# Optimization experiments

Hardware: AMD Instinct MI355X
Metric: run time of the kernel (lower is better)

Reference implementation:

```python
import jax, jax.numpy as jnp
import numpy as np

N1_SRC = 1171456  # hop-1 source nodes
N1_TGT = 45056    # hop-1 target nodes (= hop-2 source nodes)
N2_TGT = 4096     # final batch of target nodes
E1 = 1126400
E2 = 40960
IN_C, HID_C, OUT_C = 128, 256, 64


def setup_inputs() -> dict:
    key = jax.random.key(0)
    ks = jax.random.split(key, 12)
    inp = {
        "x": jax.random.normal(ks[0], (N1_SRC, IN_C), jnp.float32),
        "Wl1": jax.random.normal(ks[1], (IN_C, HID_C), jnp.float32) * (IN_C ** -0.5),
        "Wr1": jax.random.normal(ks[2], (IN_C, HID_C), jnp.float32) * (IN_C ** -0.5),
        "b1": jax.random.normal(ks[3], (HID_C,), jnp.float32) * 0.01,
        "Wl2": jax.random.normal(ks[4], (HID_C, OUT_C), jnp.float32) * (HID_C ** -0.5),
        "Wr2": jax.random.normal(ks[5], (HID_C, OUT_C), jnp.float32) * (HID_C ** -0.5),
        "b2": jax.random.normal(ks[6], (OUT_C,), jnp.float32) * 0.01,
        "src1": jax.random.randint(ks[7], (E1,), 0, N1_SRC, jnp.int32),
        "dst1": jax.random.randint(ks[8], (E1,), 0, N1_TGT, jnp.int32),
        "src2": jax.random.randint(ks[9], (E2,), 0, N1_TGT, jnp.int32),
        "dst2": jax.random.randint(ks[10], (E2,), 0, N2_TGT, jnp.int32),
    }
    return inp


def _sage_conv(x_src, x_tgt, src, dst, Wl, Wr, b, n_tgt):
    # mean aggregation of neighbor (source) features per target node
    msgs = x_src[src]                                   # [E, C] gather
    s = jax.ops.segment_sum(msgs, dst, num_segments=n_tgt)
    cnt = jax.ops.segment_sum(jnp.ones((src.shape[0],), x_src.dtype), dst,
                              num_segments=n_tgt)
    agg = s / jnp.maximum(cnt, 1.0)[:, None]
    # PyG SAGEConv: lin_l(aggregated) + lin_r(root), bias on lin_l
    return agg @ Wl + x_tgt @ Wr + b


def reference(x, Wl1, Wr1, b1, Wl2, Wr2, b2, src1, dst1, src2, dst2):
    # layer 0
    h = _sage_conv(x, x[:N1_TGT], src1, dst1, Wl1, Wr1, b1, N1_TGT)
    h = jax.nn.relu(h)  # dropout is identity in eval mode
    # layer 1
    out = _sage_conv(h, h[:N2_TGT], src2, dst2, Wl2, Wr2, b2, N2_TGT)
    return jax.nn.log_softmax(out, axis=-1)
```

## Files before the change

### kernel.cpp

```cpp
#include <hip/hip_runtime.h>
#include <hip/hip_bf16.h>

constexpr int N1_SRC = 1171456;
constexpr int N1_TGT = 45056;
constexpr int N2_TGT = 4096;
constexpr int E1 = 1126400;
constexpr int E2 = 40960;
constexpr int IN_C = 128;
constexpr int HID_C = 256;
constexpr int OUT_C = 64;

__global__ __launch_bounds__(256) void hist(const int* __restrict__ dst,
                                            int* __restrict__ cnt, int E) {
  const int i = blockIdx.x * blockDim.x + threadIdx.x;
  if (i < E) atomicAdd(&cnt[dst[i]], 1);
}

__global__ __launch_bounds__(1024) void scan_excl(const int* __restrict__ cnt,
                                                  int* __restrict__ off, int n) {
  const int tid = threadIdx.x;
  const int lane = tid & 63;
  const int wv = tid >> 6;
  __shared__ int wsum[16];
  __shared__ int carry_s;
  if (tid == 0) carry_s = 0;
  __syncthreads();
  for (int base = 0; base < n; base += 1024) {
    const int i = base + tid;
    const int v = (i < n) ? cnt[i] : 0;
    int s = v;
#pragma unroll
    for (int o = 1; o < 64; o <<= 1) {
      const int t = __shfl_up(s, o);
      if (lane >= o) s += t;
    }
    if (lane == 63) wsum[wv] = s;
    __syncthreads();
    if (wv == 0 && lane < 16) {
      const int ws = wsum[lane];
      int ss = ws;
#pragma unroll
      for (int o = 1; o < 16; o <<= 1) {
        const int t = __shfl_up(ss, o);
        if (lane >= o) ss += t;
      }
      wsum[lane] = ss - ws;
    }
    __syncthreads();
    const int excl = carry_s + wsum[wv] + (s - v);
    if (i < n) off[i] = excl;
    __syncthreads();
    if (tid == 1023) carry_s += wsum[15] + s;
    __syncthreads();
  }
}

__global__ __launch_bounds__(256) void fill_csr(
    const int* __restrict__ src, const int* __restrict__ dst,
    const int* __restrict__ off, int* __restrict__ cur,
    int* __restrict__ eidx, int E) {
  const int i = blockIdx.x * blockDim.x + threadIdx.x;
  if (i < E) {
    const int d = dst[i];
    const int p = atomicAdd(&cur[d], 1);
    eidx[off[d] + p] = src[i];
  }
}

template <int C>
__global__ __launch_bounds__(C) void gather_mean(
    const float* __restrict__ x, const int* __restrict__ eidx,
    const int* __restrict__ off, const int* __restrict__ cnt,
    float* __restrict__ agg) {
  const int node = blockIdx.x;
  const int c = threadIdx.x;
  const int beg = off[node];
  const int deg = cnt[node];
  float s0 = 0.f, s1 = 0.f, s2 = 0.f, s3 = 0.f;
  int i = 0;
  for (; i + 4 <= deg; i += 4) {
    const int n0 = eidx[beg + i + 0];
    const int n1 = eidx[beg + i + 1];
    const int n2 = eidx[beg + i + 2];
    const int n3 = eidx[beg + i + 3];
    s0 += x[(size_t)n0 * C + c];
    s1 += x[(size_t)n1 * C + c];
    s2 += x[(size_t)n2 * C + c];
    s3 += x[(size_t)n3 * C + c];
  }
  for (; i < deg; ++i) s0 += x[(size_t)eidx[beg + i] * C + c];
  const float s = (s0 + s1) + (s2 + s3);
  agg[(size_t)node * C + c] = s / (float)(deg > 0 ? deg : 1);
}

constexpr int BM = 64, BN = 64, BK = 16;
__global__ __launch_bounds__(256) void l1_dense(
    const float* __restrict__ agg1, const float* __restrict__ x,
    const float* __restrict__ Wl1, const float* __restrict__ Wr1,
    const float* __restrict__ b1, float* __restrict__ h) {
  __shared__ float As[BK][BM + 4];
  __shared__ float Bs[BK][BN + 4];
  const int br = blockIdx.x;
  const int bn = blockIdx.y;
  const int tid = threadIdx.x;
  const int tx = tid & 15;
  const int ty = tid >> 4;
  const int r0 = br * BM;
  const int n0 = bn * BN + tx * 4;

  float acc[4][4];
#pragma unroll
  for (int i = 0; i < 4; ++i)
#pragma unroll
    for (int j = 0; j < 4; ++j) acc[i][j] = b1[n0 + j];

  const int lr = tid >> 2;
  const int lk = (tid & 3) * 4;
  const int bk_ = tid >> 4;
  const int bn_ = (tid & 15) * 4;

  for (int phase = 0; phase < 2; ++phase) {
    const float* __restrict__ A = phase ? x : agg1;
    const float* __restrict__ W = phase ? Wr1 : Wl1;
    for (int k0 = 0; k0 < IN_C; k0 += BK) {
      const float4 av =
          *reinterpret_cast<const float4*>(A + (size_t)(r0 + lr) * IN_C + k0 + lk);
      As[lk + 0][lr] = av.x;
      As[lk + 1][lr] = av.y;
      As[lk + 2][lr] = av.z;
      As[lk + 3][lr] = av.w;
      const float4 wv = *reinterpret_cast<const float4*>(
          W + (size_t)(k0 + bk_) * HID_C + bn * BN + bn_);
      *reinterpret_cast<float4*>(&Bs[bk_][bn_]) = wv;
      __syncthreads();
#pragma unroll
      for (int k = 0; k < BK; ++k) {
        float a[4], b[4];
        *reinterpret_cast<float4*>(a) =
            *reinterpret_cast<const float4*>(&As[k][ty * 4]);
        *reinterpret_cast<float4*>(b) =
            *reinterpret_cast<const float4*>(&Bs[k][tx * 4]);
#pragma unroll
        for (int i = 0; i < 4; ++i)
#pragma unroll
          for (int j = 0; j < 4; ++j) acc[i][j] += a[i] * b[j];
      }
      __syncthreads();
    }
  }
#pragma unroll
  for (int i = 0; i < 4; ++i) {
    float4 o;
    o.x = fmaxf(acc[i][0], 0.0f);
    o.y = fmaxf(acc[i][1], 0.0f);
    o.z = fmaxf(acc[i][2], 0.0f);
    o.w = fmaxf(acc[i][3], 0.0f);
    *reinterpret_cast<float4*>(h + (size_t)(r0 + ty * 4 + i) * HID_C + n0) = o;
  }
}

__global__ __launch_bounds__(256) void l2_dense_lsm(
    const float* __restrict__ agg2, const float* __restrict__ h,
    const float* __restrict__ Wl2, const float* __restrict__ Wr2,
    const float* __restrict__ b2, float* __restrict__ out) {
  __shared__ float Aa[4][HID_C];
  __shared__ float Ax[4][HID_C];
  const int tid = threadIdx.x;
  const int rb = blockIdx.x * 4;
  const int lr = tid >> 6;
  const int lk = (tid & 63) * 4;
  const float4 sa =
      *reinterpret_cast<const float4*>(agg2 + (size_t)(rb + lr) * HID_C + lk);
  *reinterpret_cast<float4*>(&Aa[lr][lk]) = sa;
  const float4 xa =
      *reinterpret_cast<const float4*>(h + (size_t)(rb + lr) * HID_C + lk);
  *reinterpret_cast<float4*>(&Ax[lr][lk]) = xa;
  __syncthreads();

  const int r = tid >> 6;
  const int n = tid & 63;
  float acc = b2[n];
#pragma unroll 4
  for (int k = 0; k < HID_C; ++k) {
    acc += Aa[r][k] * Wl2[k * OUT_C + n];
    acc += Ax[r][k] * Wr2[k * OUT_C + n];
  }
  float m = acc;
#pragma unroll
  for (int o = 32; o; o >>= 1) m = fmaxf(m, __shfl_xor(m, o));
  const float e = expf(acc - m);
  float ssum = e;
#pragma unroll
  for (int o = 32; o; o >>= 1) ssum += __shfl_xor(ssum, o);
  out[(size_t)(rb + r) * OUT_C + n] = acc - m - logf(ssum);
}

extern "C" void kernel_launch(void* const* d_in, const int* in_sizes, int n_in,
                              void* d_out, int out_size, void* d_ws,
                              size_t ws_size, hipStream_t stream) {
  const float* x   = (const float*)d_in[0];
  const float* Wl1 = (const float*)d_in[1];
  const float* Wr1 = (const float*)d_in[2];
  const float* b1  = (const float*)d_in[3];
  const float* Wl2 = (const float*)d_in[4];
  const float* Wr2 = (const float*)d_in[5];
  const float* b2  = (const float*)d_in[6];
  const int* src1  = (const int*)d_in[7];
  const int* dst1  = (const int*)d_in[8];
  const int* src2  = (const int*)d_in[9];
  const int* dst2  = (const int*)d_in[10];

  int* cnt1i = (int*)d_ws;
  int* cur1  = cnt1i + N1_TGT;
  int* cnt2i = cur1 + N1_TGT;
  int* cur2  = cnt2i + N2_TGT;
  int* off1  = cur2 + N2_TGT;
  int* off2  = off1 + N1_TGT;
  int* eidx2 = off2 + N2_TGT;
  int* eidx1 = eidx2 + E2;
  float* agg1 = (float*)(eidx1 + E1);
  float* agg2 = agg1;
  float* h    = agg1 + (size_t)N1_TGT * IN_C;
  float* out  = (float*)d_out;

  hipMemsetAsync(d_ws, 0, (size_t)(2 * N1_TGT + 2 * N2_TGT) * sizeof(int),
                 stream);

  hist<<<dim3((E1 + 255) / 256), dim3(256), 0, stream>>>(dst1, cnt1i, E1);
  scan_excl<<<dim3(1), dim3(1024), 0, stream>>>(cnt1i, off1, N1_TGT);
  fill_csr<<<dim3((E1 + 255) / 256), dim3(256), 0, stream>>>(src1, dst1, off1,
                                                             cur1, eidx1, E1);
  gather_mean<IN_C><<<dim3(N1_TGT), dim3(IN_C), 0, stream>>>(x, eidx1, off1,
                                                             cnt1i, agg1);
  l1_dense<<<dim3(N1_TGT / BM, HID_C / BN), dim3(256), 0, stream>>>(
      agg1, x, Wl1, Wr1, b1, h);

  hist<<<dim3((E2 + 255) / 256), dim3(256), 0, stream>>>(dst2, cnt2i, E2);
  scan_excl<<<dim3(1), dim3(1024), 0, stream>>>(cnt2i, off2, N2_TGT);
  fill_csr<<<dim3((E2 + 255) / 256), dim3(256), 0, stream>>>(src2, dst2, off2,
                                                             cur2, eidx2, E2);
  gather_mean<HID_C><<<dim3(N2_TGT), dim3(HID_C), 0, stream>>>(h, eidx2, off2,
                                                               cnt2i, agg2);
  l2_dense_lsm<<<dim3(N2_TGT / 4), dim3(256), 0, stream>>>(agg2, h, Wl2, Wr2,
                                                           b2, out);
}
```

Baseline: 1.026 ms.

## Rewrite pipeline with bf16 MFMA layer-1 GEMM, parallel scan, and wave-per-node gathers

Replaces the fp32 SIMT layer-1 GEMM with a bf16 MFMA GEMM. The aggregated features and root features are packed into one K=256 bf16 operand with pre-transposed, concatenated weights. The single-block serial scan becomes a three-kernel multi-block scan. Gathers now use one wave per node with vectorized loads, and the hidden layer is stored as bf16 to halve its gather and read traffic. This cuts dense-compute and scan latency but adds conversion and prep kernels and introduces bf16 rounding error in the hidden activations.

```diff
diff --git a/kernel.cpp b/kernel.cpp
--- a/kernel.cpp
+++ b/kernel.cpp
@@ -9,6 +9,18 @@
 constexpr int IN_C = 128;
 constexpr int HID_C = 256;
 constexpr int OUT_C = 64;
+constexpr int KV = 256;
+
+typedef __attribute__((ext_vector_type(8))) short bf16x8;
+typedef __attribute__((ext_vector_type(4))) float f32x4;
+
+__device__ __forceinline__ unsigned f2bf(float f) {
+  unsigned u = __float_as_uint(f);
+  return (u + 0x7FFFu + ((u >> 16) & 1u)) >> 16;
+}
+__device__ __forceinline__ float bf2f(unsigned u) {
+  return __uint_as_float(u << 16);
+}
 
 __global__ __launch_bounds__(256) void hist(const int* __restrict__ dst,
                                             int* __restrict__ cnt, int E) {
@@ -16,43 +28,53 @@
   if (i < E) atomicAdd(&cnt[dst[i]], 1);
 }
 
-__global__ __launch_bounds__(1024) void scan_excl(const int* __restrict__ cnt,
-                                                  int* __restrict__ off, int n) {
-  const int tid = threadIdx.x;
-  const int lane = tid & 63;
-  const int wv = tid >> 6;
+__global__ __launch_bounds__(1024) void scan_block(const int* __restrict__ cnt,
+                                                   int* __restrict__ off,
+                                                   int* __restrict__ partials,
+                                                   int n) {
+  const int tid = threadIdx.x, lane = tid & 63, wv = tid >> 6;
   __shared__ int wsum[16];
-  __shared__ int carry_s;
-  if (tid == 0) carry_s = 0;
+  const int i = blockIdx.x * 1024 + tid;
+  const int v = (i < n) ? cnt[i] : 0;
+  int s = v;
+#pragma unroll
+  for (int o = 1; o < 64; o <<= 1) {
+    const int t = __shfl_up(s, o);
+    if (lane >= o) s += t;
+  }
+  if (lane == 63) wsum[wv] = s;
   __syncthreads();
-  for (int base = 0; base < n; base += 1024) {
-    const int i = base + tid;
-    const int v = (i < n) ? cnt[i] : 0;
-    int s = v;
-#pragma unroll
-    for (int o = 1; o < 64; o <<= 1) {
-      const int t = __shfl_up(s, o);
-      if (lane >= o) s += t;
+  if (wv == 0 && lane < 16) {
+    const int ws = wsum[lane];
+    int ss = ws;
+#pragma unroll
+    for (int o = 1; o < 16; o <<= 1) {
+      const int t = __shfl_up(ss, o);
+      if (lane >= o) ss += t;
     }
-    if (lane == 63) wsum[wv] = s;
-    __syncthreads();
-    if (wv == 0 && lane < 16) {
-      const int ws = wsum[lane];
-      int ss = ws;
-#pragma unroll
-      for (int o = 1; o < 16; o <<= 1) {
-        const int t = __shfl_up(ss, o);
-        if (lane >= o) ss += t;
-      }
-      wsum[lane] = ss - ws;
-    }
-    __syncthreads();
-    const int excl = carry_s + wsum[wv] + (s - v);
-    if (i < n) off[i] = excl;
-    __syncthreads();
-    if (tid == 1023) carry_s += wsum[15] + s;
-    __syncthreads();
-  }
+    wsum[lane] = ss - ws;
+  }
+  __syncthreads();
+  if (i < n) off[i] = wsum[wv] + s - v;
+  if (tid == 1023) partials[blockIdx.x] = wsum[15] + s;
+}
+
+__global__ __launch_bounds__(64) void scan_partials(int* __restrict__ p, int nb) {
+  const int t = threadIdx.x;
+  const int v = (t < nb) ? p[t] : 0;
+  int s = v;
+#pragma unroll
+  for (int o = 1; o < 64; o <<= 1) {
+    const int tt = __shfl_up(s, o);
+    if (t >= o) s += tt;
+  }
+  if (t < nb) p[t] = s - v;
+}
+
+__global__ __launch_bounds__(256) void scan_add(int* __restrict__ off,
+                                                const int* __restrict__ p, int n) {
+  const int i = blockIdx.x * 256 + threadIdx.x;
+  if (i < n) off[i] += p[i >> 10];
 }
 
 __global__ __launch_bounds__(256) void fill_csr(
@@ -67,132 +89,222 @@
   }
 }
 
-template <int C>
-__global__ __launch_bounds__(C) void gather_mean(
+__global__ __launch_bounds__(256) void prep_w1(const float* __restrict__ Wl1,
+                                               const float* __restrict__ Wr1,
+                                               unsigned short* __restrict__ Bt) {
+  const int idx = blockIdx.x * 256 + threadIdx.x;
+  const int k = idx & 255, n = idx >> 8;
+  const float w = (k < IN_C) ? Wl1[k * HID_C + n] : Wr1[(k - IN_C) * HID_C + n];
+  Bt[n * KV + k] = (unsigned short)f2bf(w);
+}
+
+__global__ __launch_bounds__(256) void prep_w2(const float* __restrict__ Wl2,
+                                               const float* __restrict__ Wr2,
+                                               float* __restrict__ Wl2t,
+                                               float* __restrict__ Wr2t) {
+  const int idx = blockIdx.x * 256 + threadIdx.x;
+  const int k = idx & 255, n = idx >> 8;
+  Wl2t[n * HID_C + k] = Wl2[k * OUT_C + n];
+  Wr2t[n * HID_C + k] = Wr2[k * OUT_C + n];
+}
+
+__global__ __launch_bounds__(256) void conv_x(const float* __restrict__ x,
+                                              unsigned short* __restrict__ Ab) {
+  const size_t idx = (size_t)(blockIdx.x * 256 + threadIdx.x) * 4;
+  const int m = (int)(idx >> 7);
+  const int c = (int)(idx & 127);
+  const float4 v = *reinterpret_cast<const float4*>(x + (size_t)m * IN_C + c);
+  uint2 o;
+  o.x = f2bf(v.x) | (f2bf(v.y) << 16);
+  o.y = f2bf(v.z) | (f2bf(v.w) << 16);
+  *reinterpret_cast<uint2*>(Ab + (size_t)m * KV + IN_C + c) = o;
+}
+
+__global__ __launch_bounds__(256) void gather1(
     const float* __restrict__ x, const int* __restrict__ eidx,
     const int* __restrict__ off, const int* __restrict__ cnt,
-    float* __restrict__ agg) {
-  const int node = blockIdx.x;
-  const int c = threadIdx.x;
+    unsigned short* __restrict__ Ab) {
+  const int lane = threadIdx.x & 63;
+  const int node = blockIdx.x * 4 + (threadIdx.x >> 6);
   const int beg = off[node];
   const int deg = cnt[node];
-  float s0 = 0.f, s1 = 0.f, s2 = 0.f, s3 = 0.f;
+  float s0 = 0, s1 = 0, t0 = 0, t1 = 0, u0 = 0, u1 = 0, v0 = 0, v1 = 0;
   int i = 0;
   for (; i + 4 <= deg; i += 4) {
     const int n0 = eidx[beg + i + 0];
     const int n1 = eidx[beg + i + 1];
     const int n2 = eidx[beg + i + 2];
     const int n3 = eidx[beg + i + 3];
-    s0 += x[(size_t)n0 * C + c];
-    s1 += x[(size_t)n1 * C + c];
-    s2 += x[(size_t)n2 * C + c];
-    s3 += x[(size_t)n3 * C + c];
-  }
-  for (; i < deg; ++i) s0 += x[(size_t)eidx[beg + i] * C + c];
-  const float s = (s0 + s1) + (s2 + s3);
-  agg[(size_t)node * C + c] = s / (float)(deg > 0 ? deg : 1);
-}
-
-constexpr int BM = 64, BN = 64, BK = 16;
-__global__ __launch_bounds__(256) void l1_dense(
-    const float* __restrict__ agg1, const float* __restrict__ x,
-    const float* __restrict__ Wl1, const float* __restrict__ Wr1,
-    const float* __restrict__ b1, float* __restrict__ h) {
-  __shared__ float As[BK][BM + 4];
-  __shared__ float Bs[BK][BN + 4];
-  const int br = blockIdx.x;
-  const int bn = blockIdx.y;
+    const float2 a = *reinterpret_cast<const float2*>(x + (size_t)n0 * IN_C + lane * 2);
+    const float2 b = *reinterpret_cast<const float2*>(x + (size_t)n1 * IN_C + lane * 2);
+    const float2 c = *reinterpret_cast<const float2*>(x + (size_t)n2 * IN_C + lane * 2);
+    const float2 d = *reinterpret_cast<const float2*>(x + (size_t)n3 * IN_C + lane * 2);
+    s0 += a.x; s1 += a.y; t0 += b.x; t1 += b.y;
+    u0 += c.x; u1 += c.y; v0 += d.x; v1 += d.y;
+  }
+  for (; i < deg; ++i) {
+    const int n0 = eidx[beg + i];
+    const float2 a = *reinterpret_cast<const float2*>(x + (size_t)n0 * IN_C + lane * 2);
+    s0 += a.x; s1 += a.y;
+  }
+  const float inv = 1.0f / (float)(deg > 0 ? deg : 1);
+  const float c0 = (s0 + t0 + u0 + v0) * inv;
+  const float c1 = (s1 + t1 + u1 + v1) * inv;
+  *reinterpret_cast<unsigned*>(Ab + (size_t)node * KV + lane * 2) =
+      f2bf(c0) | (f2bf(c1) << 16);
+}
+
+__global__ __launch_bounds__(256) void l1_gemm(
+    const unsigned short* __restrict__ Ab, const unsigned short* __restrict__ Bt,
+    const float* __restrict__ b1, unsigned short* __restrict__ h_bf) {
+  __shared__ unsigned short As[64 * 40];
+  __shared__ unsigned short Bs[256 * 40];
   const int tid = threadIdx.x;
-  const int tx = tid & 15;
-  const int ty = tid >> 4;
-  const int r0 = br * BM;
-  const int n0 = bn * BN + tx * 4;
-
-  float acc[4][4];
-#pragma unroll
-  for (int i = 0; i < 4; ++i)
-#pragma unroll
-    for (int j = 0; j < 4; ++j) acc[i][j] = b1[n0 + j];
-
-  const int lr = tid >> 2;
-  const int lk = (tid & 3) * 4;
-  const int bk_ = tid >> 4;
-  const int bn_ = (tid & 15) * 4;
-
-  for (int phase = 0; phase < 2; ++phase) {
-    const float* __restrict__ A = phase ? x : agg1;
-    const float* __restrict__ W = phase ? Wr1 : Wl1;
-    for (int k0 = 0; k0 < IN_C; k0 += BK) {
-      const float4 av =
-          *reinterpret_cast<const float4*>(A + (size_t)(r0 + lr) * IN_C + k0 + lk);
-      As[lk + 0][lr] = av.x;
-      As[lk + 1][lr] = av.y;
-      As[lk + 2][lr] = av.z;
-      As[lk + 3][lr] = av.w;
-      const float4 wv = *reinterpret_cast<const float4*>(
-          W + (size_t)(k0 + bk_) * HID_C + bn * BN + bn_);
-      *reinterpret_cast<float4*>(&Bs[bk_][bn_]) = wv;
-      __syncthreads();
-#pragma unroll
-      for (int k = 0; k < BK; ++k) {
-        float a[4], b[4];
-        *reinterpret_cast<float4*>(a) =
-            *reinterpret_cast<const float4*>(&As[k][ty * 4]);
-        *reinterpret_cast<float4*>(b) =
-            *reinterpret_cast<const float4*>(&Bs[k][tx * 4]);
-#pragma unroll
-        for (int i = 0; i < 4; ++i)
-#pragma unroll
-          for (int j = 0; j < 4; ++j) acc[i][j] += a[i] * b[j];
+  const int lane = tid & 63;
+  const int w = tid >> 6;
+  const int r0 = blockIdx.x * 64;
+  const int wn = w * 64;
+  f32x4 acc[4][4] = {};
+  const int arow = tid >> 2;
+  const int akoff = (tid & 3) * 8;
+  for (int ks = 0; ks < 8; ++ks) {
+    const int k0 = ks * 32;
+    if (ks) __syncthreads();
+    const bf16x8 av =
+        *reinterpret_cast<const bf16x8*>(Ab + (size_t)(r0 + arow) * KV + k0 + akoff);
+    *reinterpret_cast<bf16x8*>(As + arow * 40 + akoff) = av;
+#pragma unroll
+    for (int it = 0; it < 4; ++it) {
+      const int chunk = it * 256 + tid;
+      const int n = chunk >> 2;
+      const int koff = (chunk & 3) * 8;
+      const bf16x8 bv =
+          *reinterpret_cast<const bf16x8*>(Bt + (size_t)n * KV + k0 + koff);
+      *reinterpret_cast<bf16x8*>(Bs + n * 40 + koff) = bv;
+    }
+    __syncthreads();
+    const int kg = (lane >> 4) * 8;
+    const int rl = lane & 15;
+    bf16x8 af[4], bfr[4];
+#pragma unroll
+    for (int mi = 0; mi < 4; ++mi)
+      af[mi] = *reinterpret_cast<const bf16x8*>(As + (mi * 16 + rl) * 40 + kg);
+#pragma unroll
+    for (int nj = 0; nj < 4; ++nj)
+      bfr[nj] =
+          *reinterpret_cast<const bf16x8*>(Bs + (wn + nj * 16 + rl) * 40 + kg);
+#pragma unroll
+    for (int mi = 0; mi < 4; ++mi)
+#pragma unroll
+      for (int nj = 0; nj < 4; ++nj)
+        acc[mi][nj] = __builtin_amdgcn_mfma_f32_16x16x32_bf16(
+            af[mi], bfr[nj], acc[mi][nj], 0, 0, 0);
+  }
+  const int rl = lane & 15;
+  const int rg = lane >> 4;
+#pragma unroll
+  for (int nj = 0; nj < 4; ++nj) {
+    const int gcol = wn + nj * 16 + rl;
+    const float bias = b1[gcol];
+#pragma unroll
+    for (int mi = 0; mi < 4; ++mi)
+#pragma unroll
+      for (int r = 0; r < 4; ++r) {
+        const int grow = r0 + mi * 16 + rg * 4 + r;
+        const float v = fmaxf(acc[mi][nj][r] + bias, 0.0f);
+        h_bf[(size_t)grow * HID_C + gcol] = (unsigned short)f2bf(v);
       }
-      __syncthreads();
+  }
+}
+
+__global__ __launch_bounds__(256) void gather2(
+    const unsigned short* __restrict__ h_bf, const int* __restrict__ eidx,
+    const int* __restrict__ off, const int* __restrict__ cnt,
+    float* __restrict__ agg2) {
+  const int lane = threadIdx.x & 63;
+  const int node = blockIdx.x * 4 + (threadIdx.x >> 6);
+  const int beg = off[node];
+  const int deg = cnt[node];
+  float a0 = 0, a1 = 0, a2 = 0, a3 = 0, b0 = 0, b1v = 0, b2v = 0, b3 = 0;
+  int i = 0;
+  for (; i + 2 <= deg; i += 2) {
+    const int n0 = eidx[beg + i], n1 = eidx[beg + i + 1];
+    const uint2 ra =
+        *reinterpret_cast<const uint2*>(h_bf + (size_t)n0 * HID_C + lane * 4);
+    const uint2 rb =
+        *reinterpret_cast<const uint2*>(h_bf + (size_t)n1 * HID_C + lane * 4);
+    a0 += bf2f(ra.x & 0xffff); a1 += bf2f(ra.x >> 16);
+    a2 += bf2f(ra.y & 0xffff); a3 += bf2f(ra.y >> 16);
+    b0 += bf2f(rb.x & 0xffff); b1v += bf2f(rb.x >> 16);
+    b2v += bf2f(rb.y & 0xffff); b3 += bf2f(rb.y >> 16);
+  }
+  if (i < deg) {
+    const int n0 = eidx[beg + i];
+    const uint2 ra =
+        *reinterpret_cast<const uint2*>(h_bf + (size_t)n0 * HID_C + lane * 4);
+    a0 += bf2f(ra.x & 0xffff); a1 += bf2f(ra.x >> 16);
+    a2 += bf2f(ra.y & 0xffff); a3 += bf2f(ra.y >> 16);
+  }
+  const float inv = 1.0f / (float)(deg > 0 ? deg : 1);
+  float4 o;
+  o.x = (a0 + b0) * inv; o.y = (a1 + b1v) * inv;
+  o.z = (a2 + b2v) * inv; o.w = (a3 + b3) * inv;
+  *reinterpret_cast<float4*>(agg2 + (size_t)node * HID_C + lane * 4) = o;
+}
+
+__global__ __launch_bounds__(256) void l2_dense_lsm(
+    const float* __restrict__ agg2, const unsigned short* __restrict__ h_bf,
+    const float* __restrict__ Wl2t, const float* __restrict__ Wr2t,
+    const float* __restrict__ b2, float* __restrict__ out) {
+  __shared__ float Aa[16][HID_C];
+  __shared__ float Ax[16][HID_C];
+  const int tid = threadIdx.x;
+  const int rb = blockIdx.x * 16;
+#pragma unroll
+  for (int it = 0; it < 4; ++it) {
+    const int e = (it * 256 + tid) * 4;
+    const int row = e >> 8, c = e & 255;
+    *reinterpret_cast<float4*>(&Aa[row][c]) =
+        *reinterpret_cast<const float4*>(agg2 + (size_t)(rb + row) * HID_C + c);
+  }
+#pragma unroll
+  for (int it = 0; it < 2; ++it) {
+    const int e = (it * 256 + tid) * 8;
+    const int row = e >> 8, c = e & 255;
+    const uint4 raw =
+        *reinterpret_cast<const uint4*>(h_bf + (size_t)(rb + row) * HID_C + c);
+    Ax[row][c + 0] = bf2f(raw.x & 0xffff); Ax[row][c + 1] = bf2f(raw.x >> 16);
+    Ax[row][c + 2] = bf2f(raw.y & 0xffff); Ax[row][c + 3] = bf2f(raw.y >> 16);
+    Ax[row][c + 4] = bf2f(raw.z & 0xffff); Ax[row][c + 5] = bf2f(raw.z >> 16);
+    Ax[row][c + 6] = bf2f(raw.w & 0xffff); Ax[row][c + 7] = bf2f(raw.w >> 16);
+  }
+  __syncthreads();
+  const int n = tid & 63, rg = tid >> 6;
+  const float bias = b2[n];
+  float acc[4] = {bias, bias, bias, bias};
+  for (int k = 0; k < HID_C; k += 4) {
+    const float4 wl = *reinterpret_cast<const float4*>(Wl2t + n * HID_C + k);
+    const float4 wr = *reinterpret_cast<const float4*>(Wr2t + n * HID_C + k);
+#pragma unroll
+    for (int i = 0; i < 4; ++i) {
+      const float4 av = *reinterpret_cast<const float4*>(&Aa[rg * 4 + i][k]);
+      const float4 xv = *reinterpret_cast<const float4*>(&Ax[rg * 4 + i][k]);
+      acc[i] += av.x * wl.x + av.y * wl.y + av.z * wl.z + av.w * wl.w +
+                xv.x * wr.x + xv.y * wr.y + xv.z * wr.z + xv.w * wr.w;
     }
   }
 #pragma unroll
   for (int i = 0; i < 4; ++i) {
-    float4 o;
-    o.x = fmaxf(acc[i][0], 0.0f);
-    o.y = fmaxf(acc[i][1], 0.0f);
-    o.z = fmaxf(acc[i][2], 0.0f);
-    o.w = fmaxf(acc[i][3], 0.0f);
-    *reinterpret_cast<float4*>(h + (size_t)(r0 + ty * 4 + i) * HID_C + n0) = o;
-  }
-}
-
-__global__ __launch_bounds__(256) void l2_dense_lsm(
-    const float* __restrict__ agg2, const float* __restrict__ h,
-    const float* __restrict__ Wl2, const float* __restrict__ Wr2,
-    const float* __restrict__ b2, float* __restrict__ out) {
-  __shared__ float Aa[4][HID_C];
-  __shared__ float Ax[4][HID_C];
-  const int tid = threadIdx.x;
-  const int rb = blockIdx.x * 4;
-  const int lr = tid >> 6;
-  const int lk = (tid & 63) * 4;
-  const float4 sa =
-      *reinterpret_cast<const float4*>(agg2 + (size_t)(rb + lr) * HID_C + lk);
-  *reinterpret_cast<float4*>(&Aa[lr][lk]) = sa;
-  const float4 xa =
-      *reinterpret_cast<const float4*>(h + (size_t)(rb + lr) * HID_C + lk);
-  *reinterpret_cast<float4*>(&Ax[lr][lk]) = xa;
-  __syncthreads();
-
-  const int r = tid >> 6;
-  const int n = tid & 63;
-  float acc = b2[n];
-#pragma unroll 4
-  for (int k = 0; k < HID_C; ++k) {
-    acc += Aa[r][k] * Wl2[k * OUT_C + n];
-    acc += Ax[r][k] * Wr2[k * OUT_C + n];
-  }
-  float m = acc;
-#pragma unroll
-  for (int o = 32; o; o >>= 1) m = fmaxf(m, __shfl_xor(m, o));
-  const float e = expf(acc - m);
-  float ssum = e;
-#pragma unroll
-  for (int o = 32; o; o >>= 1) ssum += __shfl_xor(ssum, o);
-  out[(size_t)(rb + r) * OUT_C + n] = acc - m - logf(ssum);
+    const float v = acc[i];
+    float m = v;
+#pragma unroll
+    for (int o = 32; o; o >>= 1) m = fmaxf(m, __shfl_xor(m, o));
+    const float e = expf(v - m);
+    float s = e;
+#pragma unroll
+    for (int o = 32; o; o >>= 1) s += __shfl_xor(s, o);
+    out[(size_t)(rb + rg * 4 + i) * OUT_C + n] = v - m - logf(s);
+  }
 }
 
 extern "C" void kernel_launch(void* const* d_in, const int* in_sizes, int n_in,
@@ -210,37 +322,49 @@
   const int* src2  = (const int*)d_in[9];
   const int* dst2  = (const int*)d_in[10];
 
-  int* cnt1i = (int*)d_ws;
-  int* cur1  = cnt1i + N1_TGT;
-  int* cnt2i = cur1 + N1_TGT;
-  int* cur2  = cnt2i + N2_TGT;
-  int* off1  = cur2 + N2_TGT;
-  int* off2  = off1 + N1_TGT;
-  int* eidx2 = off2 + N2_TGT;
-  int* eidx1 = eidx2 + E2;
-  float* agg1 = (float*)(eidx1 + E1);
-  float* agg2 = agg1;
-  float* h    = agg1 + (size_t)N1_TGT * IN_C;
-  float* out  = (float*)d_out;
-
-  hipMemsetAsync(d_ws, 0, (size_t)(2 * N1_TGT + 2 * N2_TGT) * sizeof(int),
-                 stream);
-
-  hist<<<dim3((E1 + 255) / 256), dim3(256), 0, stream>>>(dst1, cnt1i, E1);
-  scan_excl<<<dim3(1), dim3(1024), 0, stream>>>(cnt1i, off1, N1_TGT);
+  char* p = (char*)d_ws;
+  int* cnt1 = (int*)p;                 p += (size_t)N1_TGT * 4;
+  int* cur1 = (int*)p;                 p += (size_t)N1_TGT * 4;
+  int* cnt2 = (int*)p;                 p += (size_t)N2_TGT * 4;
+  int* cur2 = (int*)p;                 p += (size_t)N2_TGT * 4;
+  const size_t zero_bytes = (size_t)(2 * N1_TGT + 2 * N2_TGT) * 4;
+  int* off1 = (int*)p;                 p += (size_t)N1_TGT * 4;
+  int* off2 = (int*)p;                 p += (size_t)N2_TGT * 4;
+  int* part1 = (int*)p;                p += 64 * 4;
+  int* part2 = (int*)p;                p += 64 * 4;
+  int* eidx1 = (int*)p;                p += (size_t)E1 * 4;
+  int* eidx2 = (int*)p;                p += (size_t)E2 * 4;
+  unsigned short* Bt = (unsigned short*)p;   p += (size_t)HID_C * KV * 2;
+  unsigned short* Ab = (unsigned short*)p;   p += (size_t)N1_TGT * KV * 2;
+  unsigned short* h_bf = (unsigned short*)p; p += (size_t)N1_TGT * HID_C * 2;
+  float* agg2 = (float*)p;             p += (size_t)N2_TGT * HID_C * 4;
+  float* Wl2t = (float*)p;             p += (size_t)OUT_C * HID_C * 4;
+  float* Wr2t = (float*)p;             p += (size_t)OUT_C * HID_C * 4;
+  float* out = (float*)d_out;
+
+  hipMemsetAsync(d_ws, 0, zero_bytes, stream);
+
+  prep_w1<<<dim3(256), dim3(256), 0, stream>>>(Wl1, Wr1, Bt);
+  prep_w2<<<dim3(64), dim3(256), 0, stream>>>(Wl2, Wr2, Wl2t, Wr2t);
+  conv_x<<<dim3(5632), dim3(256), 0, stream>>>(x, Ab);
+
+  hist<<<dim3((E1 + 255) / 256), dim3(256), 0, stream>>>(dst1, cnt1, E1);
+  scan_block<<<dim3(44), dim3(1024), 0, stream>>>(cnt1, off1, part1, N1_TGT);
+  scan_partials<<<dim3(1), dim3(64), 0, stream>>>(part1, 44);
+  scan_add<<<dim3(176), dim3(256), 0, stream>>>(off1, part1, N1_TGT);
   fill_csr<<<dim3((E1 + 255) / 256), dim3(256), 0, stream>>>(src1, dst1, off1,
                                                              cur1, eidx1, E1);
-  gather_mean<IN_C><<<dim3(N1_TGT), dim3(IN_C), 0, stream>>>(x, eidx1, off1,
-                                                             cnt1i, agg1);
-  l1_dense<<<dim3(N1_TGT / BM, HID_C / BN), dim3(256), 0, stream>>>(
-      agg1, x, Wl1, Wr1, b1, h);
-
-  hist<<<dim3((E2 + 255) / 256), dim3(256), 0, stream>>>(dst2, cnt2i, E2);
-  scan_excl<<<dim3(1), dim3(1024), 0, stream>>>(cnt2i, off2, N2_TGT);
+  gather1<<<dim3(N1_TGT / 4), dim3(256), 0, stream>>>(x, eidx1, off1, cnt1, Ab);
+  l1_gemm<<<dim3(N1_TGT / 64), dim3(256), 0, stream>>>(Ab, Bt, b1, h_bf);
+
+  hist<<<dim3((E2 + 255) / 256), dim3(256), 0, stream>>>(dst2, cnt2, E2);
+  scan_block<<<dim3(4), dim3(1024), 0, stream>>>(cnt2, off2, part2, N2_TGT);
+  scan_partials<<<dim3(1), dim3(64), 0, stream>>>(part2, 4);
+  scan_add<<<dim3(16), dim3(256), 0, stream>>>(off2, part2, N2_TGT);
   fill_csr<<<dim3((E2 + 255) / 256), dim3(256), 0, stream>>>(src2, dst2, off2,
                                                              cur2, eidx2, E2);
-  gather_mean<HID_C><<<dim3(N2_TGT), dim3(HID_C), 0, stream>>>(h, eidx2, off2,
-                                                               cnt2i, agg2);
-  l2_dense_lsm<<<dim3(N2_TGT / 4), dim3(256), 0, stream>>>(agg2, h, Wl2, Wr2,
-                                                           b2, out);
-}
+  gather2<<<dim3(N2_TGT / 4), dim3(256), 0, stream>>>(h_bf, eidx2, off2, cnt2,
+                                                      agg2);
+  l2_dense_lsm<<<dim3(N2_TGT / 16), dim3(256), 0, stream>>>(agg2, h_bf, Wl2t,
+                                                            Wr2t, b2, out);
+}
```

Result: faster. 937.1 us (-8.7%).
